# Kernel tuning notes

Hardware: AMD Instinct MI355X
Metric: run time of the kernel (lower is better)

The kernel has to match this reference:

```python
import jax, jax.numpy as jnp
import numpy as np

T, B, S = 720, 50000, 7  # timesteps, num_series, seasonality


def setup_inputs() -> dict:
    key = jax.random.key(0)
    k1, k2, k3, k4 = jax.random.split(key, 4)
    # positive data so divisions/logs are well-behaved (HW smoothing assumes positive series)
    train_padded = jax.random.uniform(k1, (T, B), jnp.float32, 0.5, 1.5)
    init_lev_sms = jax.random.uniform(k2, (B,), jnp.float32)
    init_seas_sms = jax.random.uniform(k3, (B,), jnp.float32)
    init_seasonalities = jax.random.uniform(k4, (B, S), jnp.float32)
    return {
        "train_padded": train_padded,
        "init_lev_sms": init_lev_sms,
        "init_seas_sms": init_seas_sms,
        "init_seasonalities": init_seasonalities,
    }


def _esrnn_smoothing(train_padded, init_lev_sms, init_seas_sms, init_seasonalities):
    # sigmoid of per-series smoothing params (idxs == arange(num_series))
    lev_sm = jax.nn.sigmoid(init_lev_sms)    # [B]
    seas_sm = jax.nn.sigmoid(init_seas_sms)  # [B]
    S_ = init_seasonalities.shape[1]
    init_seas = jnp.exp(init_seasonalities)  # [B, S]
    seas0_dup = init_seas[:, 0]              # seasonalities list gets exp(init[:,0]) appended again

    lev0 = train_padded[0] / init_seas[:, 0]  # [B]
    # ring buffer holding seasonalities[i .. i+S-1]; at loop start (i=1) holds indices 1..S
    buf0 = jnp.concatenate([init_seas[:, 1:].T, seas0_dup[None, :]], axis=0)  # [S, B]

    xs = (train_padded[1:], jnp.arange(1, train_padded.shape[0]))

    def step(carry, x_i):
        lev_prev, buf = carry
        x, i = x_i
        pos = (i - 1) % S_
        s_i = buf[pos]  # seasonalities[i]
        new_lev = lev_sm * (x / s_i) + (1.0 - lev_sm) * lev_prev
        log_diff = jnp.log(new_lev / lev_prev)
        new_seas = seas_sm * (x / new_lev) + (1.0 - seas_sm) * s_i  # seasonalities[i+S]
        buf = buf.at[pos].set(new_seas)
        return (new_lev, buf), (new_lev, log_diff, new_seas)

    (_, _), (levs_tail, log_diffs, seas_tail) = jax.lax.scan(step, (lev0, buf0), xs)

    levs = jnp.concatenate([lev0[None, :], levs_tail], axis=0)  # [T, B]
    seas_head = jnp.concatenate([init_seas.T, seas0_dup[None, :]], axis=0)  # [S+1, B]
    seasonalities_stacked = jnp.concatenate([seas_head, seas_tail], axis=0)  # [T+S, B]
    # level variability penalty term: mean over series of squared 2nd log-diff
    sq_log_diff = (log_diffs[1:] - log_diffs[:-1]) ** 2  # [T-2, B]
    mean_sq_log_diff = jnp.mean(sq_log_diff, axis=1)     # [T-2]
    return levs, seasonalities_stacked, mean_sq_log_diff


def reference(train_padded, init_lev_sms, init_seas_sms, init_seasonalities):
    return _esrnn_smoothing(train_padded, init_lev_sms, init_seas_sms, init_seasonalities)
```

## Files before the change

kernel.cpp:

```cpp
#include <hip/hip_runtime.h>

#define T_DIM 720
#define B_DIM 50000

#define OFF_SEAS (T_DIM * B_DIM)
#define SEAS_ROWS 727
#define OFF_MSLD (OFF_SEAS + SEAS_ROWS * B_DIM)
#define N_MSLD 718

#define NBLK 782
#define NW NBLK
#define LN2_SQ 0.4804530139182014f

__device__ __forceinline__ float dpp_sum64(float v) {
#define DPP_ADD_STAGE(CTRL, RMASK)                                             \
  v += __int_as_float(__builtin_amdgcn_update_dpp(0, __float_as_int(v),        \
                                                  CTRL, RMASK, 0xf, false));
  DPP_ADD_STAGE(0x111, 0xf)
  DPP_ADD_STAGE(0x112, 0xf)
  DPP_ADD_STAGE(0x114, 0xf)
  DPP_ADD_STAGE(0x118, 0xf)
  DPP_ADD_STAGE(0x142, 0xa)
  DPP_ADD_STAGE(0x143, 0xc)
#undef DPP_ADD_STAGE
  return v;
}

#define PREFETCH(QB, G)                                                        \
  {                                                                            \
    int tp = 1 + 7 * (G);                                                      \
    _Pragma("unroll") for (int j = 0; j < 7; ++j) {                            \
      int r = tp + j;                                                          \
      r = r > 719 ? 719 : r;                                                   \
      QB[j] = __builtin_nontemporal_load(&train[r * B_DIM + bc]);              \
    }                                                                          \
  }

#define PIN7(QB)                                                               \
  asm volatile("" : "+v"(QB[0]), "+v"(QB[1]), "+v"(QB[2]), "+v"(QB[3]),        \
                    "+v"(QB[4]), "+v"(QB[5]), "+v"(QB[6]));

#define ESRNN_GROUP_N(QB, NS)                                                  \
  {                                                                            \
    float xds[7], nlv[7], llv[7];                                              \
    _Pragma("unroll") for (int j = 0; j < (NS); ++j)                           \
        xds[j] = __fdividef(QB[j], buf[j]);                                    \
    nlv[0] = fmaf(lsm, xds[0], olm * lev);                                     \
    _Pragma("unroll") for (int j = 1; j < (NS); ++j)                           \
        nlv[j] = fmaf(lsm, xds[j], olm * nlv[j - 1]);                          \
    _Pragma("unroll") for (int j = 0; j < (NS); ++j)                           \
        llv[j] = __log2f(nlv[j]);                                              \
    _Pragma("unroll") for (int j = 0; j < (NS); ++j)                           \
        buf[j] = fmaf(ssm, __fdividef(QB[j], nlv[j]), osm * buf[j]);           \
    if (valid) {                                                               \
      _Pragma("unroll") for (int j = 0; j < (NS); ++j) {                       \
        *(float*)(lbase + boff + (unsigned)(j * B_DIM * 4)) = nlv[j];          \
        *(float*)(sbase + boff + (unsigned)(j * B_DIM * 4)) = buf[j];          \
      }                                                                        \
    }                                                                          \
    boff += (NS)*B_DIM * 4;                                                    \
    float sqv[7];                                                              \
    {                                                                          \
      float ld0 = llv[0] - llev;                                               \
      float d0 = ld0 - pld;                                                    \
      sqv[0] = valid ? d0 * d0 : 0.0f;                                         \
      float ldp = ld0;                                                         \
      _Pragma("unroll") for (int j = 1; j < (NS); ++j) {                       \
        float ld = llv[j] - llv[j - 1];                                        \
        float d = ld - ldp;                                                    \
        sqv[j] = valid ? d * d : 0.0f;                                         \
        ldp = ld;                                                              \
      }                                                                        \
      pld = ldp;                                                               \
    }                                                                          \
    llev = llv[(NS)-1];                                                        \
    lev = nlv[(NS)-1];                                                         \
    _Pragma("unroll") for (int j = 0; j < (NS); ++j)                           \
        sqv[j] = dpp_sum64(sqv[j]);                                            \
    if (lane == 63) {                                                          \
      int tb = 1 + 7 * g;                                                      \
      _Pragma("unroll") for (int j = 0; j < (NS); ++j)                         \
          lds_p[tb + j - 1] = sqv[j];                                          \
    }                                                                          \
  }

#define ESRNN_GROUP(QB, QPIN, QLD)                                             \
  {                                                                            \
    PREFETCH(QLD, g + 3)                                                       \
    PIN7(QPIN)                                                                 \
    ESRNN_GROUP_N(QB, 7)                                                       \
    ++g;                                                                       \
  }

__global__ __launch_bounds__(64) void esrnn_main(
    const float* __restrict__ train,
    const float* __restrict__ lev_sms,
    const float* __restrict__ seas_sms,
    const float* __restrict__ init_seas_in,
    float* __restrict__ levs_out,
    float* __restrict__ seas_out,
    float* __restrict__ partial)
{
  __shared__ float lds_p[720];

  int b = blockIdx.x * 64 + threadIdx.x;
  bool valid = (b < B_DIM);
  int bc = valid ? b : (B_DIM - 1);
  int lane = threadIdx.x;
  int wid = blockIdx.x;

  float lsm = 1.0f / (1.0f + __expf(-lev_sms[bc]));
  float ssm = 1.0f / (1.0f + __expf(-seas_sms[bc]));
  float olm = 1.0f - lsm;
  float osm = 1.0f - ssm;

  float is[7];
#pragma unroll
  for (int j = 0; j < 7; ++j) is[j] = __expf(init_seas_in[bc * 7 + j]);

  float seas0 = is[0];
  float x0 = train[bc];
  float lev = __fdividef(x0, seas0);

  if (valid) {
    levs_out[b] = lev;
#pragma unroll
    for (int j = 0; j < 7; ++j) seas_out[j * B_DIM + b] = is[j];
    seas_out[7 * B_DIM + b] = seas0;
  }

  float buf[7];
#pragma unroll
  for (int j = 0; j < 6; ++j) buf[j] = is[j + 1];
  buf[6] = seas0;

  float llev = __log2f(lev);
  float pld = 0.0f;

  char* lbase = (char*)levs_out + (size_t)B_DIM * 4;
  char* sbase = (char*)seas_out + (size_t)8 * B_DIM * 4;
  unsigned int boff = (unsigned int)b * 4u;

  float xa[7], xb[7], xc[7], xd[7];
  int g = 0;
  PREFETCH(xa, 0)
  PREFETCH(xb, 1)
  PREFETCH(xc, 2)

  for (int k = 0; k < 25; ++k) {
    ESRNN_GROUP(xa, xb, xd)
    ESRNN_GROUP(xb, xc, xa)
    ESRNN_GROUP(xc, xd, xb)
    ESRNN_GROUP(xd, xa, xc)
  }
  ESRNN_GROUP(xa, xb, xd)
  ESRNN_GROUP(xb, xc, xa)

  ESRNN_GROUP_N(xc, 5)

  __syncthreads();
  float* mystrip = partial + (size_t)wid * N_MSLD;
  for (int i = lane; i < N_MSLD; i += 64) mystrip[i] = lds_p[i + 1];
}

__global__ __launch_bounds__(64) void esrnn_reduce2(
    const float* __restrict__ partial, float* __restrict__ msld) {
  int row = blockIdx.x;
  int lane = threadIdx.x;
  float s = 0.0f;
  for (int i = lane; i < NW; i += 64)
    s += partial[(size_t)i * N_MSLD + row];
  float tot = dpp_sum64(s);
  if (lane == 63) msld[row] = tot * (LN2_SQ / (float)B_DIM);
}

extern "C" void kernel_launch(void* const* d_in, const int* in_sizes, int n_in,
                              void* d_out, int out_size, void* d_ws,
                              size_t ws_size, hipStream_t stream) {
  const float* train = (const float*)d_in[0];
  const float* lev_sms = (const float*)d_in[1];
  const float* seas_sms = (const float*)d_in[2];
  const float* init_seas = (const float*)d_in[3];

  float* out = (float*)d_out;
  float* levs = out;
  float* seas = out + OFF_SEAS;
  float* msld = out + OFF_MSLD;
  float* partial = (float*)d_ws;

  esrnn_main<<<NBLK, 64, 0, stream>>>(train, lev_sms, seas_sms, init_seas,
                                      levs, seas, partial);
  esrnn_reduce2<<<N_MSLD, 64, 0, stream>>>(partial, msld);
}
```

Measured before the change: 116.5 us.

## Split recurrence and output/log work across producer and consumer wavefronts

Each block now has two wavefronts. Wave 0 runs only the level and seasonality recurrence and writes each group's results into a double-buffered LDS tile. Wave 1 reads that tile one group later and handles the log2, the global stores of levels and seasonalities, and the squared-log-diff DPP reductions. The aim is to take transcendental, store and reduction work off the serial critical path so the two can overlap. In exchange it adds a block barrier per group, LDS traffic, and twice the threads per block.

After: 129.5 us. 11.2% more time.

```diff
diff --git a/kernel.cpp b/kernel.cpp
--- a/kernel.cpp
+++ b/kernel.cpp
@@ -4,13 +4,14 @@
 #define B_DIM 50000
 
 #define OFF_SEAS (T_DIM * B_DIM)
-#define SEAS_ROWS 727
-#define OFF_MSLD (OFF_SEAS + SEAS_ROWS * B_DIM)
+#define OFF_MSLD (OFF_SEAS + 727 * B_DIM)
 #define N_MSLD 718
 
 #define NBLK 782
 #define NW NBLK
 #define LN2_SQ 0.4804530139182014f
+
+typedef float v2f __attribute__((ext_vector_type(2)));
 
 __device__ __forceinline__ float dpp_sum64(float v) {
 #define DPP_ADD_STAGE(CTRL, RMASK)                                             \
@@ -26,6 +27,10 @@
   return v;
 }
 
+#define PIN7(QB)                                                               \
+  asm volatile("" : "+v"(QB[0]), "+v"(QB[1]), "+v"(QB[2]), "+v"(QB[3]),        \
+                    "+v"(QB[4]), "+v"(QB[5]), "+v"(QB[6]));
+
 #define PREFETCH(QB, G)                                                        \
   {                                                                            \
     int tp = 1 + 7 * (G);                                                      \
@@ -36,30 +41,43 @@
     }                                                                          \
   }
 
-#define PIN7(QB)                                                               \
-  asm volatile("" : "+v"(QB[0]), "+v"(QB[1]), "+v"(QB[2]), "+v"(QB[3]),        \
-                    "+v"(QB[4]), "+v"(QB[5]), "+v"(QB[6]));
-
-#define ESRNN_GROUP_N(QB, NS)                                                  \
+#define W0C(QB, NS)                                                            \
   {                                                                            \
-    float xds[7], nlv[7], llv[7];                                              \
+    float xds[7], nlv[7];                                                      \
     _Pragma("unroll") for (int j = 0; j < (NS); ++j)                           \
         xds[j] = __fdividef(QB[j], buf[j]);                                    \
     nlv[0] = fmaf(lsm, xds[0], olm * lev);                                     \
     _Pragma("unroll") for (int j = 1; j < (NS); ++j)                           \
         nlv[j] = fmaf(lsm, xds[j], olm * nlv[j - 1]);                          \
     _Pragma("unroll") for (int j = 0; j < (NS); ++j)                           \
-        llv[j] = __log2f(nlv[j]);                                              \
-    _Pragma("unroll") for (int j = 0; j < (NS); ++j)                           \
         buf[j] = fmaf(ssm, __fdividef(QB[j], nlv[j]), osm * buf[j]);           \
+    _Pragma("unroll") for (int j = 0; j < (NS); ++j) {                         \
+      v2f p;                                                                   \
+      p.x = nlv[j];                                                            \
+      p.y = buf[j];                                                            \
+      dbuf[g & 1][j][lane] = p;                                                \
+    }                                                                          \
+    lev = nlv[(NS)-1];                                                         \
+    ++g;                                                                       \
+  }
+
+#define W1P(NS)                                                                \
+  {                                                                            \
+    float nl[7], nsv[7], llv[7], sqv[7];                                       \
+    _Pragma("unroll") for (int j = 0; j < (NS); ++j) {                         \
+      v2f p = dbuf[qcnt & 1][j][lane];                                         \
+      nl[j] = p.x;                                                             \
+      nsv[j] = p.y;                                                            \
+    }                                                                          \
+    _Pragma("unroll") for (int j = 0; j < (NS); ++j)                           \
+        llv[j] = __log2f(nl[j]);                                               \
     if (valid) {                                                               \
       _Pragma("unroll") for (int j = 0; j < (NS); ++j) {                       \
-        *(float*)(lbase + boff + (unsigned)(j * B_DIM * 4)) = nlv[j];          \
-        *(float*)(sbase + boff + (unsigned)(j * B_DIM * 4)) = buf[j];          \
+        *(float*)(lbase + boff + (unsigned)(j * B_DIM * 4)) = nl[j];           \
+        *(float*)(sbase + boff + (unsigned)(j * B_DIM * 4)) = nsv[j];          \
       }                                                                        \
     }                                                                          \
     boff += (NS)*B_DIM * 4;                                                    \
-    float sqv[7];                                                              \
     {                                                                          \
       float ld0 = llv[0] - llev;                                               \
       float d0 = ld0 - pld;                                                    \
@@ -74,93 +92,99 @@
       pld = ldp;                                                               \
     }                                                                          \
     llev = llv[(NS)-1];                                                        \
-    lev = nlv[(NS)-1];                                                         \
     _Pragma("unroll") for (int j = 0; j < (NS); ++j)                           \
         sqv[j] = dpp_sum64(sqv[j]);                                            \
     if (lane == 63) {                                                          \
-      int tb = 1 + 7 * g;                                                      \
+      int tb = 1 + 7 * qcnt;                                                   \
       _Pragma("unroll") for (int j = 0; j < (NS); ++j)                         \
           lds_p[tb + j - 1] = sqv[j];                                          \
     }                                                                          \
-  }
-
-#define ESRNN_GROUP(QB, QPIN, QLD)                                             \
-  {                                                                            \
-    PREFETCH(QLD, g + 3)                                                       \
-    PIN7(QPIN)                                                                 \
-    ESRNN_GROUP_N(QB, 7)                                                       \
-    ++g;                                                                       \
-  }
-
-__global__ __launch_bounds__(64) void esrnn_main(
-    const float* __restrict__ train,
-    const float* __restrict__ lev_sms,
-    const float* __restrict__ seas_sms,
-    const float* __restrict__ init_seas_in,
-    float* __restrict__ levs_out,
-    float* __restrict__ seas_out,
-    float* __restrict__ partial)
-{
+    ++qcnt;                                                                    \
+  }
+
+__global__ __launch_bounds__(128) void esrnn_main(
+    const float* __restrict__ train, const float* __restrict__ lev_sms,
+    const float* __restrict__ seas_sms, const float* __restrict__ init_seas_in,
+    float* __restrict__ levs_out, float* __restrict__ seas_out,
+    float* __restrict__ partial) {
+  __shared__ v2f dbuf[2][7][64];
   __shared__ float lds_p[720];
 
-  int b = blockIdx.x * 64 + threadIdx.x;
+  int tid = threadIdx.x;
+  int lane = tid & 63;
+  int w = tid >> 6;
+  int wid = blockIdx.x;
+  int b = wid * 64 + lane;
   bool valid = (b < B_DIM);
   int bc = valid ? b : (B_DIM - 1);
-  int lane = threadIdx.x;
-  int wid = blockIdx.x;
-
-  float lsm = 1.0f / (1.0f + __expf(-lev_sms[bc]));
-  float ssm = 1.0f / (1.0f + __expf(-seas_sms[bc]));
-  float olm = 1.0f - lsm;
-  float osm = 1.0f - ssm;
-
-  float is[7];
-#pragma unroll
-  for (int j = 0; j < 7; ++j) is[j] = __expf(init_seas_in[bc * 7 + j]);
-
-  float seas0 = is[0];
-  float x0 = train[bc];
-  float lev = __fdividef(x0, seas0);
-
-  if (valid) {
-    levs_out[b] = lev;
-#pragma unroll
-    for (int j = 0; j < 7; ++j) seas_out[j * B_DIM + b] = is[j];
-    seas_out[7 * B_DIM + b] = seas0;
-  }
-
+
+  float lsm = 0, olm = 0, ssm = 0, osm = 0, lev = 0;
   float buf[7];
-#pragma unroll
-  for (int j = 0; j < 6; ++j) buf[j] = is[j + 1];
-  buf[6] = seas0;
-
-  float llev = __log2f(lev);
-  float pld = 0.0f;
-
+  float xa[7], xb[7], xc[7], xd[7];
+  int g = 0;
+  float llev = 0, pld = 0;
+  unsigned boff = 0;
+  int qcnt = 0;
   char* lbase = (char*)levs_out + (size_t)B_DIM * 4;
   char* sbase = (char*)seas_out + (size_t)8 * B_DIM * 4;
-  unsigned int boff = (unsigned int)b * 4u;
-
-  float xa[7], xb[7], xc[7], xd[7];
-  int g = 0;
-  PREFETCH(xa, 0)
-  PREFETCH(xb, 1)
-  PREFETCH(xc, 2)
-
-  for (int k = 0; k < 25; ++k) {
-    ESRNN_GROUP(xa, xb, xd)
-    ESRNN_GROUP(xb, xc, xa)
-    ESRNN_GROUP(xc, xd, xb)
-    ESRNN_GROUP(xd, xa, xc)
-  }
-  ESRNN_GROUP(xa, xb, xd)
-  ESRNN_GROUP(xb, xc, xa)
-
-  ESRNN_GROUP_N(xc, 5)
-
-  __syncthreads();
-  float* mystrip = partial + (size_t)wid * N_MSLD;
-  for (int i = lane; i < N_MSLD; i += 64) mystrip[i] = lds_p[i + 1];
+
+  if (w == 0) {
+    lsm = 1.0f / (1.0f + __expf(-lev_sms[bc]));
+    ssm = 1.0f / (1.0f + __expf(-seas_sms[bc]));
+    olm = 1.0f - lsm;
+    osm = 1.0f - ssm;
+    float is[7];
+#pragma unroll
+    for (int j = 0; j < 7; ++j) is[j] = __expf(init_seas_in[bc * 7 + j]);
+    lev = __fdividef(train[bc], is[0]);
+#pragma unroll
+    for (int j = 0; j < 6; ++j) buf[j] = is[j + 1];
+    buf[6] = is[0];
+    PREFETCH(xa, 0)
+    PREFETCH(xb, 1)
+    PREFETCH(xc, 2)
+  } else {
+    float is[7];
+#pragma unroll
+    for (int j = 0; j < 7; ++j) is[j] = __expf(init_seas_in[bc * 7 + j]);
+    float lev0 = __fdividef(train[bc], is[0]);
+    llev = __log2f(lev0);
+    pld = 0.0f;
+    boff = (unsigned)b * 4u;
+    if (valid) {
+      levs_out[b] = lev0;
+#pragma unroll
+      for (int j = 0; j < 7; ++j) seas_out[j * B_DIM + b] = is[j];
+      seas_out[7 * B_DIM + b] = is[0];
+    }
+  }
+
+  if (w == 0) {
+    PREFETCH(xd, 3)
+    PIN7(xb)
+    W0C(xa, 7)
+  }
+  __syncthreads();
+
+  for (int kk = 0; kk < 25; ++kk) {
+    if (w == 0) { PREFETCH(xa, g + 3) PIN7(xc) W0C(xb, 7) } else { W1P(7) }
+    __syncthreads();
+    if (w == 0) { PREFETCH(xb, g + 3) PIN7(xd) W0C(xc, 7) } else { W1P(7) }
+    __syncthreads();
+    if (w == 0) { PREFETCH(xc, g + 3) PIN7(xa) W0C(xd, 7) } else { W1P(7) }
+    __syncthreads();
+    if (w == 0) { PREFETCH(xd, g + 3) PIN7(xb) W0C(xa, 7) } else { W1P(7) }
+    __syncthreads();
+  }
+  if (w == 0) { PIN7(xc) W0C(xb, 7) } else { W1P(7) }
+  __syncthreads();
+  if (w == 0) { W0C(xc, 5) } else { W1P(7) }
+  __syncthreads();
+  if (w == 1) { W1P(5) }
+  __syncthreads();
+
+  for (int i = tid; i < N_MSLD; i += 128)
+    partial[(size_t)wid * N_MSLD + i] = lds_p[i + 1];
 }
 
 __global__ __launch_bounds__(64) void esrnn_reduce2(
@@ -168,8 +192,7 @@
   int row = blockIdx.x;
   int lane = threadIdx.x;
   float s = 0.0f;
-  for (int i = lane; i < NW; i += 64)
-    s += partial[(size_t)i * N_MSLD + row];
+  for (int i = lane; i < NW; i += 64) s += partial[(size_t)i * N_MSLD + row];
   float tot = dpp_sum64(s);
   if (lane == 63) msld[row] = tot * (LN2_SQ / (float)B_DIM);
 }
@@ -188,7 +211,7 @@
   float* msld = out + OFF_MSLD;
   float* partial = (float*)d_ws;
 
-  esrnn_main<<<NBLK, 64, 0, stream>>>(train, lev_sms, seas_sms, init_seas,
-                                      levs, seas, partial);
+  esrnn_main<<<NBLK, 128, 0, stream>>>(train, lev_sms, seas_sms, init_seas,
+                                       levs, seas, partial);
   esrnn_reduce2<<<N_MSLD, 64, 0, stream>>>(partial, msld);
 }
```

## Process two series per thread with float2 vector loads and stores

Applied to the files above, without the earlier changes.

Each thread now handles a pair of adjacent series using float2 vectors, which halves the block count to 391 and turns the global loads and stores into 8-byte accesses. The aim is better instruction-level parallelism from two independent recurrences per thread, packed FMA and sub ops, and fewer memory instructions. The cost is half as many wavefronts for hiding latency on a device with many CUs, plus higher register pressure from the doubled prefetch buffers.

New measurement: 146.4 us. 1.26x slower.

```diff
diff --git a/kernel.cpp b/kernel.cpp
--- a/kernel.cpp
+++ b/kernel.cpp
@@ -4,13 +4,15 @@
 #define B_DIM 50000
 
 #define OFF_SEAS (T_DIM * B_DIM)
-#define SEAS_ROWS 727
-#define OFF_MSLD (OFF_SEAS + SEAS_ROWS * B_DIM)
+#define OFF_MSLD (OFF_SEAS + 727 * B_DIM)
 #define N_MSLD 718
 
-#define NBLK 782
+#define NPAIR 25000
+#define NBLK 391
 #define NW NBLK
 #define LN2_SQ 0.4804530139182014f
+
+typedef float v2f __attribute__((ext_vector_type(2)));
 
 __device__ __forceinline__ float dpp_sum64(float v) {
 #define DPP_ADD_STAGE(CTRL, RMASK)                                             \
@@ -26,49 +28,64 @@
   return v;
 }
 
+__device__ __forceinline__ v2f v2div(v2f a, v2f b) {
+  v2f r;
+  r.x = __fdividef(a.x, b.x);
+  r.y = __fdividef(a.y, b.y);
+  return r;
+}
+__device__ __forceinline__ v2f v2log2(v2f a) {
+  v2f r;
+  r.x = __log2f(a.x);
+  r.y = __log2f(a.y);
+  return r;
+}
+
+#define PIN7(QB)                                                               \
+  asm volatile("" : "+v"(QB[0]), "+v"(QB[1]), "+v"(QB[2]), "+v"(QB[3]),        \
+                    "+v"(QB[4]), "+v"(QB[5]), "+v"(QB[6]));
+
 #define PREFETCH(QB, G)                                                        \
   {                                                                            \
     int tp = 1 + 7 * (G);                                                      \
     _Pragma("unroll") for (int j = 0; j < 7; ++j) {                            \
       int r = tp + j;                                                          \
       r = r > 719 ? 719 : r;                                                   \
-      QB[j] = __builtin_nontemporal_load(&train[r * B_DIM + bc]);              \
-    }                                                                          \
-  }
-
-#define PIN7(QB)                                                               \
-  asm volatile("" : "+v"(QB[0]), "+v"(QB[1]), "+v"(QB[2]), "+v"(QB[3]),        \
-                    "+v"(QB[4]), "+v"(QB[5]), "+v"(QB[6]));
+      QB[j] = __builtin_nontemporal_load(                                      \
+          (const v2f*)((const char*)train + (size_t)r * B_DIM * 4 +            \
+                       8ull * (unsigned)pc));                                  \
+    }                                                                          \
+  }
 
 #define ESRNN_GROUP_N(QB, NS)                                                  \
   {                                                                            \
-    float xds[7], nlv[7], llv[7];                                              \
-    _Pragma("unroll") for (int j = 0; j < (NS); ++j)                           \
-        xds[j] = __fdividef(QB[j], buf[j]);                                    \
-    nlv[0] = fmaf(lsm, xds[0], olm * lev);                                     \
+    v2f xds[7], nlv[7], llv[7];                                                \
+    _Pragma("unroll") for (int j = 0; j < (NS); ++j)                           \
+        xds[j] = v2div(QB[j], buf[j]);                                         \
+    nlv[0] = lsm2 * xds[0] + olm2 * lev;                                       \
     _Pragma("unroll") for (int j = 1; j < (NS); ++j)                           \
-        nlv[j] = fmaf(lsm, xds[j], olm * nlv[j - 1]);                          \
-    _Pragma("unroll") for (int j = 0; j < (NS); ++j)                           \
-        llv[j] = __log2f(nlv[j]);                                              \
-    _Pragma("unroll") for (int j = 0; j < (NS); ++j)                           \
-        buf[j] = fmaf(ssm, __fdividef(QB[j], nlv[j]), osm * buf[j]);           \
+        nlv[j] = lsm2 * xds[j] + olm2 * nlv[j - 1];                            \
+    _Pragma("unroll") for (int j = 0; j < (NS); ++j)                           \
+        llv[j] = v2log2(nlv[j]);                                               \
+    _Pragma("unroll") for (int j = 0; j < (NS); ++j)                           \
+        buf[j] = ssm2 * v2div(QB[j], nlv[j]) + osm2 * buf[j];                  \
     if (valid) {                                                               \
       _Pragma("unroll") for (int j = 0; j < (NS); ++j) {                       \
-        *(float*)(lbase + boff + (unsigned)(j * B_DIM * 4)) = nlv[j];          \
-        *(float*)(sbase + boff + (unsigned)(j * B_DIM * 4)) = buf[j];          \
+        *(v2f*)(lbase + boff + (unsigned)(j * B_DIM * 4)) = nlv[j];            \
+        *(v2f*)(sbase + boff + (unsigned)(j * B_DIM * 4)) = buf[j];            \
       }                                                                        \
     }                                                                          \
     boff += (NS)*B_DIM * 4;                                                    \
     float sqv[7];                                                              \
     {                                                                          \
-      float ld0 = llv[0] - llev;                                               \
-      float d0 = ld0 - pld;                                                    \
-      sqv[0] = valid ? d0 * d0 : 0.0f;                                         \
-      float ldp = ld0;                                                         \
+      v2f ld0 = llv[0] - llev;                                                 \
+      v2f d0 = ld0 - pld;                                                      \
+      sqv[0] = valid ? (d0.x * d0.x + d0.y * d0.y) : 0.0f;                     \
+      v2f ldp = ld0;                                                           \
       _Pragma("unroll") for (int j = 1; j < (NS); ++j) {                       \
-        float ld = llv[j] - llv[j - 1];                                        \
-        float d = ld - ldp;                                                    \
-        sqv[j] = valid ? d * d : 0.0f;                                         \
+        v2f ld = llv[j] - llv[j - 1];                                          \
+        v2f d = ld - ldp;                                                      \
+        sqv[j] = valid ? (d.x * d.x + d.y * d.y) : 0.0f;                       \
         ldp = ld;                                                              \
       }                                                                        \
       pld = ldp;                                                               \
@@ -103,45 +120,57 @@
 {
   __shared__ float lds_p[720];
 
-  int b = blockIdx.x * 64 + threadIdx.x;
-  bool valid = (b < B_DIM);
-  int bc = valid ? b : (B_DIM - 1);
   int lane = threadIdx.x;
   int wid = blockIdx.x;
-
-  float lsm = 1.0f / (1.0f + __expf(-lev_sms[bc]));
-  float ssm = 1.0f / (1.0f + __expf(-seas_sms[bc]));
-  float olm = 1.0f - lsm;
-  float osm = 1.0f - ssm;
-
-  float is[7];
+  int p = wid * 64 + lane;
+  bool valid = (p < NPAIR);
+  int pc = valid ? p : (NPAIR - 1);
+
+  v2f lraw = *(const v2f*)&lev_sms[2 * pc];
+  v2f sraw = *(const v2f*)&seas_sms[2 * pc];
+  v2f lsm2, ssm2;
+  lsm2.x = 1.0f / (1.0f + __expf(-lraw.x));
+  lsm2.y = 1.0f / (1.0f + __expf(-lraw.y));
+  ssm2.x = 1.0f / (1.0f + __expf(-sraw.x));
+  ssm2.y = 1.0f / (1.0f + __expf(-sraw.y));
+  v2f olm2 = 1.0f - lsm2;
+  v2f osm2 = 1.0f - ssm2;
+
+  v2f isv[7];
 #pragma unroll
-  for (int j = 0; j < 7; ++j) is[j] = __expf(init_seas_in[bc * 7 + j]);
-
-  float seas0 = is[0];
-  float x0 = train[bc];
-  float lev = __fdividef(x0, seas0);
+  for (int j = 0; j < 7; ++j) {
+    isv[j].x = __expf(init_seas_in[pc * 14 + j]);
+    isv[j].y = __expf(init_seas_in[pc * 14 + 7 + j]);
+  }
+
+  v2f x0 = *(const v2f*)((const char*)train + 8ull * (unsigned)pc);
+  v2f lev = v2div(x0, isv[0]);
 
   if (valid) {
-    levs_out[b] = lev;
+    *(v2f*)&levs_out[2 * p] = lev;
 #pragma unroll
-    for (int j = 0; j < 7; ++j) seas_out[j * B_DIM + b] = is[j];
-    seas_out[7 * B_DIM + b] = seas0;
-  }
-
-  float buf[7];
+    for (int j = 0; j < 7; ++j)
+      *(v2f*)((char*)seas_out + (size_t)j * B_DIM * 4 + 8ull * (unsigned)p) =
+          isv[j];
+    *(v2f*)((char*)seas_out + (size_t)7 * B_DIM * 4 + 8ull * (unsigned)p) =
+        isv[0];
+  }
+
+  v2f buf[7];
 #pragma unroll
-  for (int j = 0; j < 6; ++j) buf[j] = is[j + 1];
-  buf[6] = seas0;
-
-  float llev = __log2f(lev);
-  float pld = 0.0f;
+  for (int j = 0; j < 6; ++j) buf[j] = isv[j + 1];
+  buf[6] = isv[0];
+
+  v2f llev = v2log2(lev);
+  v2f pld;
+  pld.x = 0.0f;
+  pld.y = 0.0f;
 
   char* lbase = (char*)levs_out + (size_t)B_DIM * 4;
   char* sbase = (char*)seas_out + (size_t)8 * B_DIM * 4;
-  unsigned int boff = (unsigned int)b * 4u;
-
-  float xa[7], xb[7], xc[7], xd[7];
+  unsigned boff = 8u * (unsigned)p;
+
+  v2f xa[7], xb[7], xc[7], xd[7];
   int g = 0;
   PREFETCH(xa, 0)
   PREFETCH(xb, 1)
@@ -168,8 +197,7 @@
   int row = blockIdx.x;
   int lane = threadIdx.x;
   float s = 0.0f;
-  for (int i = lane; i < NW; i += 64)
-    s += partial[(size_t)i * N_MSLD + row];
+  for (int i = lane; i < NW; i += 64) s += partial[(size_t)i * N_MSLD + row];
   float tot = dpp_sum64(s);
   if (lane == 63) msld[row] = tot * (LN2_SQ / (float)B_DIM);
 }
```
